# Kernel optimization log

Hardware: AMD Instinct MI355X
Metric: run time of the kernel (lower is better)

## Reference

```python
import jax, jax.numpy as jnp
import numpy as np

B, N, K = 4, 4096, 16
D_IN, D_T = 64, 128


def _linear_params(key, d_in, d_out, scale=0.02):
    kw, kb = jax.random.split(key)
    w = jax.random.normal(kw, (d_in, d_out), dtype=jnp.float32) * scale
    b = jax.random.normal(kb, (d_out,), dtype=jnp.float32) * scale
    return w, b


def setup_inputs() -> dict:
    key = jax.random.key(0)
    ks = jax.random.split(key, 12)
    x = jax.random.normal(ks[0], (B, N, D_IN), dtype=jnp.float32)
    pos = jax.random.normal(ks[1], (B, N, 3), dtype=jnp.float32)
    fc1_w, fc1_b = _linear_params(ks[2], D_IN, D_T)
    fc2_w, fc2_b = _linear_params(ks[3], D_T, D_IN)
    d1_w, d1_b = _linear_params(ks[4], 3, D_T)
    d2_w, d2_b = _linear_params(ks[5], D_T, D_T)
    g1_w, g1_b = _linear_params(ks[6], D_T, D_T)
    g2_w, g2_b = _linear_params(ks[7], D_T, D_T)
    wq = jax.random.normal(ks[8], (D_T, D_T), dtype=jnp.float32) * 0.02
    wk = jax.random.normal(ks[9], (D_T, D_T), dtype=jnp.float32) * 0.02
    wv = jax.random.normal(ks[10], (D_T, D_T), dtype=jnp.float32) * 0.02
    return dict(x=x, pos=pos, fc1_w=fc1_w, fc1_b=fc1_b, fc2_w=fc2_w, fc2_b=fc2_b,
                d1_w=d1_w, d1_b=d1_b, d2_w=d2_w, d2_b=d2_b,
                g1_w=g1_w, g1_b=g1_b, g2_w=g2_w, g2_b=g2_b,
                wq=wq, wk=wk, wv=wv)


def reference(x, pos, fc1_w, fc1_b, fc2_w, fc2_b, d1_w, d1_b, d2_w, d2_b,
              g1_w, g1_b, g2_w, g2_b, wq, wk, wv):
    # square_distance(pos, pos): [B, N, N]
    sq = jnp.sum(pos * pos, axis=-1)
    dists = sq[:, :, None] + sq[:, None, :] - 2.0 * jnp.einsum('bnc,bmc->bnm', pos, pos)
    knn_idx = jnp.argsort(dists, axis=-1)[:, :, :K]  # [B, N, K] int
    bidx = jnp.arange(B)[:, None, None]

    knn_pos = pos[bidx, knn_idx]                     # [B, N, K, 3]
    h = x @ fc1_w + fc1_b                            # [B, N, D_T]
    q = h @ wq                                       # [B, N, D_T]
    k = (h @ wk)[bidx, knn_idx]                      # [B, N, K, D_T]
    v = (h @ wv)[bidx, knn_idx]                      # [B, N, K, D_T]

    rel = pos[:, :, None, :] - knn_pos               # [B, N, K, 3]
    pos_enc = jax.nn.relu(rel @ d1_w + d1_b) @ d2_w + d2_b  # fc_delta

    a_in = q[:, :, None, :] - k + pos_enc
    attn = jax.nn.relu(a_in @ g1_w + g1_b) @ g2_w + g2_b    # fc_gamma
    attn = jax.nn.softmax(attn / np.sqrt(D_T).astype(np.float32), axis=-2)

    res = jnp.einsum('bmnf,bmnf->bmf', attn, v + pos_enc)   # [B, N, D_T]
    out = res @ fc2_w + fc2_b + x                           # [B, N, D_IN]
    return out, attn
```

## Files before the change

### kernel.cpp

```cpp
#include <hip/hip_runtime.h>
#include <float.h>

#define NPTS 4096
#define BN   16384
#define DT   128
#define DIN  64

typedef short v8s __attribute__((ext_vector_type(8)));
typedef float v4f __attribute__((ext_vector_type(4)));

__device__ __forceinline__ unsigned short f2bf(float f) {
    union { float f; unsigned u; } v; v.f = f;
    unsigned r = v.u + 0x7fff + ((v.u >> 16) & 1);
    return (unsigned short)(r >> 16);
}
__device__ __forceinline__ float bf2f(unsigned short s) {
    union { unsigned u; float f; } v; v.u = ((unsigned)s) << 16;
    return v.f;
}
__device__ __forceinline__ unsigned pack2(float lo, float hi) {
    unsigned r;
    asm("v_cvt_pk_bf16_f32 %0, %1, %2" : "=v"(r) : "v"(lo), "v"(hi));
    return r;
}

#define CSW(da,ia,db,ib) { bool sw_ = (da>db)||((da==db)&&(ia>ib)); \
    float td_=sw_?db:da, tD_=sw_?da:db; int ti_=sw_?ib:ia, tI_=sw_?ia:ib; \
    da=td_; db=tD_; ia=ti_; ib=tI_; }

__global__ __launch_bounds__(256) void front_kernel(
    const float* __restrict__ pos, const float* __restrict__ x,
    const float* __restrict__ fc1w, const float* __restrict__ fc1b,
    const float* __restrict__ wq, const float* __restrict__ wk,
    const float* __restrict__ wv,
    const float* __restrict__ d2w, const float* __restrict__ g1w,
    const float* __restrict__ g2w,
    float4* __restrict__ pos4, unsigned short* __restrict__ wB,
    int* __restrict__ knnb,
    unsigned short* __restrict__ qb, unsigned short* __restrict__ kb,
    unsigned short* __restrict__ vb) {
    __shared__ float smem[4096];
    int bid = blockIdx.x;
    int t = threadIdx.x;

    if (bid < 2048) {
        float (*scd)[256] = (float(*)[256])smem;
        int   (*sci)[256] = (int(*)[256])(smem + 2048);
        int lane = t & 63, w = t >> 6;
        int n0 = bid * 8 + w * 2;
        int base = n0 & ~(NPTS - 1);
        float pax = pos[n0*3], pay = pos[n0*3+1], paz = pos[n0*3+2];
        float paw = fmaf(paz, paz, fmaf(pay, pay, pax*pax));
        float pbx = pos[n0*3+3], pby = pos[n0*3+4], pbz = pos[n0*3+5];
        float pbw = fmaf(pbz, pbz, fmaf(pby, pby, pbx*pbx));

        float mina = FLT_MAX, minb = FLT_MAX;
        for (int m = lane; m < NPTS; m += 64) {
            const float* cp = &pos[(size_t)(base + m)*3];
            float cx = cp[0], cy = cp[1], cz = cp[2];
            float cw = fmaf(cz, cz, fmaf(cy, cy, cx*cx));
            float da = (paw + cw) - 2.0f * fmaf(paz, cz, fmaf(pay, cy, pax*cx));
            float db = (pbw + cw) - 2.0f * fmaf(pbz, cz, fmaf(pby, cy, pbx*cx));
            mina = fminf(mina, da); minb = fminf(minb, db);
        }
        float taua, taub;
        {
            float va = mina, vb_ = minb;
#pragma unroll
            for (int k = 2; k <= 64; k <<= 1) {
#pragma unroll
                for (int j = k >> 1; j > 0; j >>= 1) {
                    float oa = __shfl_xor(va, j, 64);
                    float ob = __shfl_xor(vb_, j, 64);
                    bool low = (lane & j) == 0;
                    bool asc = (lane & k) == 0;
                    va  = (low == asc) ? fminf(va, oa)  : fmaxf(va, oa);
                    vb_ = (low == asc) ? fminf(vb_, ob) : fmaxf(vb_, ob);
                }
            }
            taua = __shfl(va, 15, 64);
            taub = __shfl(vb_, 15, 64);
        }
        int ca = 0, cb = 0;
        for (int m = lane; m < NPTS; m += 64) {
            const float* cp = &pos[(size_t)(base + m)*3];
            float cx = cp[0], cy = cp[1], cz = cp[2];
            float cw = fmaf(cz, cz, fmaf(cy, cy, cx*cx));
            float da = (paw + cw) - 2.0f * fmaf(paz, cz, fmaf(pay, cy, pax*cx));
            float db = (pbw + cw) - 2.0f * fmaf(pbz, cz, fmaf(pby, cy, pbx*cx));
            bool ta = da <= taua, tb_ = db <= taub;
            unsigned long long ma = __ballot(ta), mb = __ballot(tb_);
            unsigned long long lower = (1ull << lane) - 1ull;
            if (ta) {
                int p_ = ca + __popcll(ma & lower);
                if (p_ < 256) { scd[w*2][p_] = da; sci[w*2][p_] = base + m; }
            }
            if (tb_) {
                int p_ = cb + __popcll(mb & lower);
                if (p_ < 256) { scd[w*2+1][p_] = db; sci[w*2+1][p_] = base + m; }
            }
            ca += __popcll(ma); cb += __popcll(mb);
        }
        if (ca > 256) ca = 256;
        if (cb > 256) cb = 256;
        for (int i = ca + lane; i < 256; i += 64) { scd[w*2][i]   = FLT_MAX; sci[w*2][i]   = 0x7fffffff; }
        for (int i = cb + lane; i < 256; i += 64) { scd[w*2+1][i] = FLT_MAX; sci[w*2+1][i] = 0x7fffffff; }
        __syncthreads();

        for (int pt = 0; pt < 2; pt++) {
            int s = w*2 + pt;
            float4 dv = *(const float4*)&scd[s][lane*4];
            int4   iv = *(const int4*)&sci[s][lane*4];
            CSW(dv.x, iv.x, dv.y, iv.y);
            CSW(dv.z, iv.z, dv.w, iv.w);
            CSW(dv.x, iv.x, dv.z, iv.z);
            CSW(dv.y, iv.y, dv.w, iv.w);
            CSW(dv.y, iv.y, dv.z, iv.z);
            int p = 0, myres = 0;
            for (int r = 0; r < 16; r++) {
                float hd = p==0 ? dv.x : p==1 ? dv.y : p==2 ? dv.z : p==3 ? dv.w : FLT_MAX;
                int   hi = p==0 ? iv.x : p==1 ? iv.y : p==2 ? iv.z : p==3 ? iv.w : 0x7fffffff;
                float bd = hd; int bi = hi;
                for (int off = 32; off; off >>= 1) {
                    float od = __shfl_xor(bd, off, 64);
                    int   oi = __shfl_xor(bi, off, 64);
                    if (od < bd || (od == bd && oi < bi)) { bd = od; bi = oi; }
                }
                if (hi == bi) p++;
                if (lane == r) myres = bi;
            }
            if (lane < 16) knnb[(n0 + pt)*16 + lane] = myres;
        }
    } else if (bid < 3072) {
        float (*xs)[64]  = (float(*)[64])smem;
        float (*hs)[128] = (float(*)[128])(smem + 1024);
        int rb = (bid - 2048) * 16;

        for (int i = t; i < 16*64; i += 256) xs[i>>6][i&63] = x[rb*64 + i];
        __syncthreads();

        int f4 = (t & 31) * 4;
        int r0 = (t >> 5) * 2, r1 = r0 + 1;
        float a0[4], a1[4];
#pragma unroll
        for (int jf = 0; jf < 4; jf++) { a0[jf] = fc1b[f4+jf]; a1[jf] = fc1b[f4+jf]; }
#pragma unroll 4
        for (int c = 0; c < 64; c += 4) {
            float s0[4], s1[4];
            *(float4*)s0 = *(const float4*)&xs[r0][c];
            *(float4*)s1 = *(const float4*)&xs[r1][c];
#pragma unroll
            for (int jc = 0; jc < 4; jc++) {
                float w[4];
                *(float4*)w = *(const float4*)&fc1w[(c+jc)*128 + f4];
#pragma unroll
                for (int jf = 0; jf < 4; jf++) {
                    a0[jf] = fmaf(s0[jc], w[jf], a0[jf]);
                    a1[jf] = fmaf(s1[jc], w[jf], a1[jf]);
                }
            }
        }
        *(float4*)&hs[r0][f4] = *(float4*)a0;
        *(float4*)&hs[r1][f4] = *(float4*)a1;
        __syncthreads();

        const float* Ws[3] = { wq, wk, wv };
        unsigned short* Os[3] = { qb, kb, vb };
        for (int mtx = 0; mtx < 3; mtx++) {
            const float* __restrict__ W = Ws[mtx];
#pragma unroll
            for (int jf = 0; jf < 4; jf++) { a0[jf] = 0.f; a1[jf] = 0.f; }
#pragma unroll 4
            for (int c = 0; c < 128; c += 4) {
                float s0[4], s1[4];
                *(float4*)s0 = *(const float4*)&hs[r0][c];
                *(float4*)s1 = *(const float4*)&hs[r1][c];
#pragma unroll
                for (int jc = 0; jc < 4; jc++) {
                    float w[4];
                    *(float4*)w = *(const float4*)&W[(c+jc)*128 + f4];
#pragma unroll
                    for (int jf = 0; jf < 4; jf++) {
                        a0[jf] = fmaf(s0[jc], w[jf], a0[jf]);
                        a1[jf] = fmaf(s1[jc], w[jf], a1[jf]);
                    }
                }
            }
            unsigned short* O = Os[mtx];
            uint2 s0v, s1v;
            s0v.x = pack2(a0[0], a0[1]); s0v.y = pack2(a0[2], a0[3]);
            s1v.x = pack2(a1[0], a1[1]); s1v.y = pack2(a1[2], a1[3]);
            *(uint2*)&O[(size_t)(rb+r0)*128 + f4] = s0v;
            *(uint2*)&O[(size_t)(rb+r1)*128 + f4] = s1v;
        }
    } else {
        int i = (bid - 3072) * 256 + t;
        if (i < BN) {
            float p0 = pos[i*3], p1 = pos[i*3+1], p2 = pos[i*3+2];
            pos4[i] = make_float4(p0, p1, p2, fmaf(p2, p2, fmaf(p1, p1, p0*p0)));
        } else {
            int e = i - BN; int m = e >> 14; e &= 16383;
            int k = e >> 7, n = e & 127;
            const float* W = (m == 0) ? d2w : (m == 1) ? g1w : g2w;
            float val = W[k*128 + n];
            int tile = n >> 4, nl = n & 15, ks = k >> 5, q = (k >> 3) & 3, j = k & 7;
            wB[m*16384 + ((tile*4 + ks)*64 + q*16 + nl)*8 + j] = f2bf(val);
        }
    }
}

__global__ __attribute__((amdgpu_waves_per_eu(4, 4)))
__launch_bounds__(1024) void fused_kernel(
    const float4* __restrict__ pos4, const int* __restrict__ knnb,
    const unsigned short* __restrict__ qb, const unsigned short* __restrict__ kb,
    const unsigned short* __restrict__ vb,
    const unsigned short* __restrict__ wB,
    const float* __restrict__ d1w, const float* __restrict__ d1b,
    const float* __restrict__ d2b, const float* __restrict__ g1b,
    const float* __restrict__ g2b,
    float* __restrict__ res, float* __restrict__ attn) {
    __shared__ unsigned short ws_[49152];
    __shared__ unsigned short tb[16][2048];
    int t = threadIdx.x;
    int lane = t & 63, w = t >> 6;
    int col = lane & 15, quad = lane >> 4;
    const float inv_s = 0.08838834764831845f;

    unsigned short* tw = &tb[w][0];
    float* twf = (float*)tw;

    {
        const uint4* src = (const uint4*)wB;
        uint4* dst = (uint4*)ws_;
        for (int i = t; i < 6144; i += 1024) dst[i] = src[i];
    }
    __syncthreads();

#pragma unroll
    for (int it = 0; it < 2; it++) {
        int n = (blockIdx.x * 16 + w) * 2 + it;
        {
            int jid = knnb[n*16 + col];

#pragma unroll
            for (int g = 0; g < 4; g++) {
                int kk2 = quad*4 + g;
                int jr2 = __shfl(jid, kk2);
                v8s kr = *(const v8s*)&kb[(size_t)jr2*128 + col*8];
                *(v8s*)&tw[kk2*128 + ((col ^ (kk2 & 7)) << 3)] = kr;
            }

            float4 pn = pos4[n];
            float4 pj = pos4[jid];
            float dx = pn.x - pj.x, dy = pn.y - pj.y, dz = pn.z - pj.z;

            v8s af[4];
#pragma unroll
            for (int ks = 0; ks < 4; ks++) {
                int fb = ks*32 + quad*8;
                float w0[8], w1[8], w2[8], bb[8];
                *(float4*)&w0[0] = *(const float4*)&d1w[fb];
                *(float4*)&w0[4] = *(const float4*)&d1w[fb+4];
                *(float4*)&w1[0] = *(const float4*)&d1w[128+fb];
                *(float4*)&w1[4] = *(const float4*)&d1w[128+fb+4];
                *(float4*)&w2[0] = *(const float4*)&d1w[256+fb];
                *(float4*)&w2[4] = *(const float4*)&d1w[256+fb+4];
                *(float4*)&bb[0] = *(const float4*)&d1b[fb];
                *(float4*)&bb[4] = *(const float4*)&d1b[fb+4];
                union { v8s s; unsigned u[4]; } afu;
#pragma unroll
                for (int j2 = 0; j2 < 4; j2++) {
                    float h0 = fmaf(dz, w2[j2*2],   fmaf(dy, w1[j2*2],   fmaf(dx, w0[j2*2],   bb[j2*2])));
                    float h1 = fmaf(dz, w2[j2*2+1], fmaf(dy, w1[j2*2+1], fmaf(dx, w0[j2*2+1], bb[j2*2+1])));
                    afu.u[j2] = pack2(fmaxf(h0, 0.0f), fmaxf(h1, 0.0f));
                }
                af[ks] = afu.s;
            }

            v8s frag[4];
            unsigned peP[16];

            {
                unsigned wo = 0; asm volatile("" : "+v"(wo));
#pragma unroll
                for (int tt = 0; tt < 8; tt++) {
                    v4f acc = {0.f, 0.f, 0.f, 0.f};
#pragma unroll
                    for (int ks = 0; ks < 4; ks++) {
                        v8s b = *(const v8s*)&ws_[wo + ((tt*4 + ks) << 9) + (lane << 3)];
                        acc = __builtin_amdgcn_mfma_f32_16x16x32_bf16(af[ks], b, acc, 0, 0, 0);
                    }
                    int cg = tt*16 + col;
                    float bias = d2b[cg];
                    float qv = bf2f(qb[(size_t)n*128 + cg]);
                    float pe0 = 0.f, pe1 = 0.f;
#pragma unroll
                    for (int r = 0; r < 4; r++) {
                        int kk = quad*4 + r;
                        int pidx = kk*128 + ((((cg >> 3) ^ (kk & 7))) << 3) + (cg & 6);
                        unsigned kp = *(const unsigned*)&tw[pidx];
                        float kv = bf2f((unsigned short)((lane & 1) ? (kp >> 16) : (kp & 0xffff)));
                        float pe = acc[r] + bias;
                        if (r == 0) pe0 = pe;
                        if (r == 1) { peP[tt*2]   = pack2(pe0, pe); }
                        if (r == 2) pe1 = pe;
                        if (r == 3) { peP[tt*2+1] = pack2(pe1, pe); }
                        float a  = qv - kv + pe;
                        float o = __shfl_xor(a, 1);
                        if ((lane & 1) == 0) *(unsigned*)&tw[pidx] = pack2(a, o);
                    }
                }
#pragma unroll
                for (int ks = 0; ks < 4; ks++)
                    frag[ks] = *(const v8s*)&tw[col*128 + ((((ks*4 + quad) ^ (col & 7))) << 3)];
            }

            {
                unsigned wo = 16384; asm volatile("" : "+v"(wo));
#pragma unroll
                for (int tt = 0; tt < 8; tt++) {
                    v4f acc = {0.f, 0.f, 0.f, 0.f};
#pragma unroll
                    for (int ks = 0; ks < 4; ks++) {
                        v8s b = *(const v8s*)&ws_[wo + ((tt*4 + ks) << 9) + (lane << 3)];
                        acc = __builtin_amdgcn_mfma_f32_16x16x32_bf16(frag[ks], b, acc, 0, 0, 0);
                    }
                    float bias = g1b[tt*16 + col];
#pragma unroll
                    for (int r = 0; r < 4; r++) {
                        float h = fmaxf(acc[r] + bias, 0.0f);
                        float o = __shfl_xor(h, 1);
                        if ((lane & 1) == 0) {
                            int kk = quad*4 + r;
                            int cg = tt*16 + col;
                            int idx = kk*128 + ((((cg >> 3) ^ (kk & 7))) << 3) + (cg & 7);
                            *(unsigned*)&tw[idx] = pack2(h, o);
                        }
                    }
                }
#pragma unroll
                for (int ks = 0; ks < 4; ks++)
                    frag[ks] = *(const v8s*)&tw[col*128 + ((((ks*4 + quad) ^ (col & 7))) << 3)];
            }

            {
#pragma unroll
                for (int g = 0; g < 4; g++) {
                    int kk2 = quad*4 + g;
                    int jr2 = __shfl(jid, kk2);
                    v8s vr = *(const v8s*)&vb[(size_t)jr2*128 + col*8];
                    *(v8s*)&tw[kk2*128 + ((col ^ (kk2 & 7)) << 3)] = vr;
                }

                unsigned wo = 32768; asm volatile("" : "+v"(wo));
                float av[8][4];
#pragma unroll
                for (int tt = 0; tt < 8; tt++) {
                    v4f acc = {0.f, 0.f, 0.f, 0.f};
#pragma unroll
                    for (int ks = 0; ks < 4; ks++) {
                        v8s b = *(const v8s*)&ws_[wo + ((tt*4 + ks) << 9) + (lane << 3)];
                        acc = __builtin_amdgcn_mfma_f32_16x16x32_bf16(frag[ks], b, acc, 0, 0, 0);
                    }
                    int cg = tt*16 + col;
                    float bias = g2b[cg];
                    float l[4];
                    float mx = -FLT_MAX;
#pragma unroll
                    for (int r = 0; r < 4; r++) {
                        l[r] = (acc[r] + bias) * inv_s;
                        mx = fmaxf(mx, l[r]);
                    }
                    mx = fmaxf(mx, __shfl_xor(mx, 16));
                    mx = fmaxf(mx, __shfl_xor(mx, 32));
                    float s = 0.f;
#pragma unroll
                    for (int r = 0; r < 4; r++) { l[r] = __expf(l[r] - mx); s += l[r]; }
                    s += __shfl_xor(s, 16);
                    s += __shfl_xor(s, 32);
                    float rs = 1.0f / s;
                    float rp = 0.f;
#pragma unroll
                    for (int r = 0; r < 4; r++) {
                        int kk = quad*4 + r;
                        int pidx = kk*128 + ((((cg >> 3) ^ (kk & 7))) << 3) + (cg & 6);
                        unsigned vp = *(const unsigned*)&tw[pidx];
                        float vv = bf2f((unsigned short)((lane & 1) ? (vp >> 16) : (vp & 0xffff)));
                        unsigned pp = peP[tt*2 + (r >> 1)];
                        float pe = bf2f((unsigned short)((r & 1) ? (pp >> 16) : (pp & 0xffff)));
                        float a_ = l[r] * rs;
                        av[tt][r] = a_;
                        rp = fmaf(a_, vv + pe, rp);
                    }
                    rp += __shfl_xor(rp, 16);
                    rp += __shfl_xor(rp, 32);
                    if (lane < 16) res[(size_t)n*128 + cg] = rp;
                }

#pragma unroll
                for (int h = 0; h < 2; h++) {
#pragma unroll
                    for (int tt2 = 0; tt2 < 4; tt2++) {
#pragma unroll
                        for (int r = 0; r < 4; r++) {
                            int kk = quad*4 + r;
                            twf[kk*64 + ((tt2*16 + col) ^ ((kk & 4) << 2))] = av[h*4 + tt2][r];
                        }
                    }
#pragma unroll
                    for (int s4 = 0; s4 < 4; s4++) {
                        int kk = s4*4 + quad;
                        int c4 = col*4;
                        float4 a4 = *(const float4*)&twf[kk*64 + (c4 ^ ((kk & 4) << 2))];
                        *(float4*)&attn[(size_t)(n*16 + kk)*128 + h*64 + c4] = a4;
                    }
                }
            }
        }
    }
}

__global__ __launch_bounds__(256) void epi_kernel(
    const float* __restrict__ res, const float* __restrict__ fc2w,
    const float* __restrict__ fc2b, const float* __restrict__ x,
    float* __restrict__ out) {
    __shared__ float fw[128][64];
    __shared__ float rs[16][128];
    int t = threadIdx.x;
    int rb = blockIdx.x * 16;
    for (int i = t; i < 8192; i += 256) fw[i >> 6][i & 63] = fc2w[i];
    for (int i = t; i < 2048; i += 256) rs[i >> 7][i & 127] = res[(size_t)rb*128 + i];
    __syncthreads();

    int o = t & 63, g = t >> 6;
#pragma unroll
    for (int rr = 0; rr < 4; rr++) {
        int lr = rr*4 + g;
        int n = rb + lr;
        float a0 = 0.f, a1 = 0.f, a2 = 0.f, a3 = 0.f;
#pragma unroll 8
        for (int c = 0; c < 128; c += 4) {
            a0 = fmaf(rs[lr][c],   fw[c][o],   a0);
            a1 = fmaf(rs[lr][c+1], fw[c+1][o], a1);
            a2 = fmaf(rs[lr][c+2], fw[c+2][o], a2);
            a3 = fmaf(rs[lr][c+3], fw[c+3][o], a3);
        }
        out[(size_t)n*64 + o] = (a0 + a1) + (a2 + a3) + fc2b[o] + x[(size_t)n*64 + o];
    }
}

extern "C" void kernel_launch(void* const* d_in, const int* in_sizes, int n_in,
                              void* d_out, int out_size, void* d_ws, size_t ws_size,
                              hipStream_t stream) {
    (void)in_sizes; (void)n_in; (void)out_size; (void)ws_size;
    const float* x    = (const float*)d_in[0];
    const float* pos  = (const float*)d_in[1];
    const float* fc1w = (const float*)d_in[2];
    const float* fc1b = (const float*)d_in[3];
    const float* fc2w = (const float*)d_in[4];
    const float* fc2b = (const float*)d_in[5];
    const float* d1w  = (const float*)d_in[6];
    const float* d1b  = (const float*)d_in[7];
    const float* d2w  = (const float*)d_in[8];
    const float* d2b  = (const float*)d_in[9];
    const float* g1w  = (const float*)d_in[10];
    const float* g1b  = (const float*)d_in[11];
    const float* g2w  = (const float*)d_in[12];
    const float* g2b  = (const float*)d_in[13];
    const float* wq   = (const float*)d_in[14];
    const float* wk   = (const float*)d_in[15];
    const float* wv   = (const float*)d_in[16];

    float* out      = (float*)d_out;
    float* attn_out = out + (size_t)BN * DIN;

    char* W = (char*)d_ws;
    float4*         pos4  = (float4*)(W + 0);
    unsigned short* wB    = (unsigned short*)(W + 262144);
    int*            knnb  = (int*)(W + 376832);
    unsigned short* qb    = (unsigned short*)(W + 1441792);
    unsigned short* kb    = (unsigned short*)(W + 5636096);
    unsigned short* vb    = (unsigned short*)(W + 9830400);
    float*          res   = (float*)(W + 14024704);

    front_kernel<<<3328, 256, 0, stream>>>(pos, x, fc1w, fc1b, wq, wk, wv,
                                           d2w, g1w, g2w,
                                           pos4, wB, knnb, qb, kb, vb);
    fused_kernel<<<512, 1024, 0, stream>>>(pos4, knnb, qb, kb, vb, wB, d1w, d1b,
                                           d2b, g1b, g2b, res, attn_out);
    epi_kernel<<<1024, 256, 0, stream>>>(res, fc2w, fc2b, x, out);
}
```

Measured before the change: 435.8 us.

## Split KNN into own kernel and stage candidate positions in LDS

Moves the KNN search out of the combined front kernel into a dedicated kernel, with the remaining front work in a separate launch. Each KNN block first loads all 4096 batch positions into shared memory as float4 with precomputed squared norm, so the two scan passes read LDS instead of strided global loads and recompute no norms. This costs 64KB of LDS per block, which limits occupancy, and adds an extra kernel launch.

```diff
diff --git a/kernel.cpp b/kernel.cpp
--- a/kernel.cpp
+++ b/kernel.cpp
@@ -28,7 +28,102 @@
     float td_=sw_?db:da, tD_=sw_?da:db; int ti_=sw_?ib:ia, tI_=sw_?ia:ib; \
     da=td_; db=tD_; ia=ti_; ib=tI_; }
 
-__global__ __launch_bounds__(256) void front_kernel(
+__global__ __launch_bounds__(256) void knn_kernel(const float* __restrict__ pos,
+                                                  int* __restrict__ knnb) {
+    __shared__ float4 pc[NPTS];
+    __shared__ float scd[8][256];
+    __shared__ int   sci[8][256];
+    int t = threadIdx.x, lane = t & 63, w = t >> 6;
+    int n0 = blockIdx.x * 8 + w * 2;
+    int base = n0 & ~(NPTS - 1);
+
+    for (int p = t; p < NPTS; p += 256) {
+        const float* cp = &pos[(size_t)(base + p)*3];
+        float cx = cp[0], cy = cp[1], cz = cp[2];
+        pc[p] = make_float4(cx, cy, cz, fmaf(cz, cz, fmaf(cy, cy, cx*cx)));
+    }
+
+    float pax = pos[n0*3], pay = pos[n0*3+1], paz = pos[n0*3+2];
+    float paw = fmaf(paz, paz, fmaf(pay, pay, pax*pax));
+    float pbx = pos[n0*3+3], pby = pos[n0*3+4], pbz = pos[n0*3+5];
+    float pbw = fmaf(pbz, pbz, fmaf(pby, pby, pbx*pbx));
+    __syncthreads();
+
+    float mina = FLT_MAX, minb = FLT_MAX;
+    for (int m = lane; m < NPTS; m += 64) {
+        float4 c = pc[m];
+        float da = (paw + c.w) - 2.0f * fmaf(paz, c.z, fmaf(pay, c.y, pax*c.x));
+        float db = (pbw + c.w) - 2.0f * fmaf(pbz, c.z, fmaf(pby, c.y, pbx*c.x));
+        mina = fminf(mina, da); minb = fminf(minb, db);
+    }
+    float taua, taub;
+    {
+        float va = mina, vb_ = minb;
+#pragma unroll
+        for (int k = 2; k <= 64; k <<= 1) {
+#pragma unroll
+            for (int j = k >> 1; j > 0; j >>= 1) {
+                float oa = __shfl_xor(va, j, 64);
+                float ob = __shfl_xor(vb_, j, 64);
+                bool low = (lane & j) == 0;
+                bool asc = (lane & k) == 0;
+                va  = (low == asc) ? fminf(va, oa)  : fmaxf(va, oa);
+                vb_ = (low == asc) ? fminf(vb_, ob) : fmaxf(vb_, ob);
+            }
+        }
+        taua = __shfl(va, 15, 64);
+        taub = __shfl(vb_, 15, 64);
+    }
+    int ca = 0, cb = 0;
+    for (int m = lane; m < NPTS; m += 64) {
+        float4 c = pc[m];
+        float da = (paw + c.w) - 2.0f * fmaf(paz, c.z, fmaf(pay, c.y, pax*c.x));
+        float db = (pbw + c.w) - 2.0f * fmaf(pbz, c.z, fmaf(pby, c.y, pbx*c.x));
+        bool ta = da <= taua, tb_ = db <= taub;
+        unsigned long long ma = __ballot(ta), mb = __ballot(tb_);
+        unsigned long long lower = (1ull << lane) - 1ull;
+        if (ta) {
+            int p_ = ca + __popcll(ma & lower);
+            if (p_ < 256) { scd[w*2][p_] = da; sci[w*2][p_] = base + m; }
+        }
+        if (tb_) {
+            int p_ = cb + __popcll(mb & lower);
+            if (p_ < 256) { scd[w*2+1][p_] = db; sci[w*2+1][p_] = base + m; }
+        }
+        ca += __popcll(ma); cb += __popcll(mb);
+    }
+    if (ca > 256) ca = 256;
+    if (cb > 256) cb = 256;
+    for (int i = ca + lane; i < 256; i += 64) { scd[w*2][i]   = FLT_MAX; sci[w*2][i]   = 0x7fffffff; }
+    for (int i = cb + lane; i < 256; i += 64) { scd[w*2+1][i] = FLT_MAX; sci[w*2+1][i] = 0x7fffffff; }
+
+    for (int pt = 0; pt < 2; pt++) {
+        int s = w*2 + pt;
+        float4 dv = *(const float4*)&scd[s][lane*4];
+        int4   iv = *(const int4*)&sci[s][lane*4];
+        CSW(dv.x, iv.x, dv.y, iv.y);
+        CSW(dv.z, iv.z, dv.w, iv.w);
+        CSW(dv.x, iv.x, dv.z, iv.z);
+        CSW(dv.y, iv.y, dv.w, iv.w);
+        CSW(dv.y, iv.y, dv.z, iv.z);
+        int p = 0, myres = 0;
+        for (int r = 0; r < 16; r++) {
+            float hd = p==0 ? dv.x : p==1 ? dv.y : p==2 ? dv.z : p==3 ? dv.w : FLT_MAX;
+            int   hi = p==0 ? iv.x : p==1 ? iv.y : p==2 ? iv.z : p==3 ? iv.w : 0x7fffffff;
+            float bd = hd; int bi = hi;
+            for (int off = 32; off; off >>= 1) {
+                float od = __shfl_xor(bd, off, 64);
+                int   oi = __shfl_xor(bi, off, 64);
+                if (od < bd || (od == bd && oi < bi)) { bd = od; bi = oi; }
+            }
+            if (hi == bi) p++;
+            if (lane == r) myres = bi;
+        }
+        if (lane < 16) knnb[(n0 + pt)*16 + lane] = myres;
+    }
+}
+
+__global__ __launch_bounds__(256) void fp_kernel(
     const float* __restrict__ pos, const float* __restrict__ x,
     const float* __restrict__ fc1w, const float* __restrict__ fc1b,
     const float* __restrict__ wq, const float* __restrict__ wk,
@@ -36,105 +131,16 @@
     const float* __restrict__ d2w, const float* __restrict__ g1w,
     const float* __restrict__ g2w,
     float4* __restrict__ pos4, unsigned short* __restrict__ wB,
-    int* __restrict__ knnb,
     unsigned short* __restrict__ qb, unsigned short* __restrict__ kb,
     unsigned short* __restrict__ vb) {
-    __shared__ float smem[4096];
+    __shared__ float smem[3072];
     int bid = blockIdx.x;
     int t = threadIdx.x;
 
-    if (bid < 2048) {
-        float (*scd)[256] = (float(*)[256])smem;
-        int   (*sci)[256] = (int(*)[256])(smem + 2048);
-        int lane = t & 63, w = t >> 6;
-        int n0 = bid * 8 + w * 2;
-        int base = n0 & ~(NPTS - 1);
-        float pax = pos[n0*3], pay = pos[n0*3+1], paz = pos[n0*3+2];
-        float paw = fmaf(paz, paz, fmaf(pay, pay, pax*pax));
-        float pbx = pos[n0*3+3], pby = pos[n0*3+4], pbz = pos[n0*3+5];
-        float pbw = fmaf(pbz, pbz, fmaf(pby, pby, pbx*pbx));
-
-        float mina = FLT_MAX, minb = FLT_MAX;
-        for (int m = lane; m < NPTS; m += 64) {
-            const float* cp = &pos[(size_t)(base + m)*3];
-            float cx = cp[0], cy = cp[1], cz = cp[2];
-            float cw = fmaf(cz, cz, fmaf(cy, cy, cx*cx));
-            float da = (paw + cw) - 2.0f * fmaf(paz, cz, fmaf(pay, cy, pax*cx));
-            float db = (pbw + cw) - 2.0f * fmaf(pbz, cz, fmaf(pby, cy, pbx*cx));
-            mina = fminf(mina, da); minb = fminf(minb, db);
-        }
-        float taua, taub;
-        {
-            float va = mina, vb_ = minb;
-#pragma unroll
-            for (int k = 2; k <= 64; k <<= 1) {
-#pragma unroll
-                for (int j = k >> 1; j > 0; j >>= 1) {
-                    float oa = __shfl_xor(va, j, 64);
-                    float ob = __shfl_xor(vb_, j, 64);
-                    bool low = (lane & j) == 0;
-                    bool asc = (lane & k) == 0;
-                    va  = (low == asc) ? fminf(va, oa)  : fmaxf(va, oa);
-                    vb_ = (low == asc) ? fminf(vb_, ob) : fmaxf(vb_, ob);
-                }
-            }
-            taua = __shfl(va, 15, 64);
-            taub = __shfl(vb_, 15, 64);
-        }
-        int ca = 0, cb = 0;
-        for (int m = lane; m < NPTS; m += 64) {
-            const float* cp = &pos[(size_t)(base + m)*3];
-            float cx = cp[0], cy = cp[1], cz = cp[2];
-            float cw = fmaf(cz, cz, fmaf(cy, cy, cx*cx));
-            float da = (paw + cw) - 2.0f * fmaf(paz, cz, fmaf(pay, cy, pax*cx));
-            float db = (pbw + cw) - 2.0f * fmaf(pbz, cz, fmaf(pby, cy, pbx*cx));
-            bool ta = da <= taua, tb_ = db <= taub;
-            unsigned long long ma = __ballot(ta), mb = __ballot(tb_);
-            unsigned long long lower = (1ull << lane) - 1ull;
-            if (ta) {
-                int p_ = ca + __popcll(ma & lower);
-                if (p_ < 256) { scd[w*2][p_] = da; sci[w*2][p_] = base + m; }
-            }
-            if (tb_) {
-                int p_ = cb + __popcll(mb & lower);
-                if (p_ < 256) { scd[w*2+1][p_] = db; sci[w*2+1][p_] = base + m; }
-            }
-            ca += __popcll(ma); cb += __popcll(mb);
-        }
-        if (ca > 256) ca = 256;
-        if (cb > 256) cb = 256;
-        for (int i = ca + lane; i < 256; i += 64) { scd[w*2][i]   = FLT_MAX; sci[w*2][i]   = 0x7fffffff; }
-        for (int i = cb + lane; i < 256; i += 64) { scd[w*2+1][i] = FLT_MAX; sci[w*2+1][i] = 0x7fffffff; }
-        __syncthreads();
-
-        for (int pt = 0; pt < 2; pt++) {
-            int s = w*2 + pt;
-            float4 dv = *(const float4*)&scd[s][lane*4];
-            int4   iv = *(const int4*)&sci[s][lane*4];
-            CSW(dv.x, iv.x, dv.y, iv.y);
-            CSW(dv.z, iv.z, dv.w, iv.w);
-            CSW(dv.x, iv.x, dv.z, iv.z);
-            CSW(dv.y, iv.y, dv.w, iv.w);
-            CSW(dv.y, iv.y, dv.z, iv.z);
-            int p = 0, myres = 0;
-            for (int r = 0; r < 16; r++) {
-                float hd = p==0 ? dv.x : p==1 ? dv.y : p==2 ? dv.z : p==3 ? dv.w : FLT_MAX;
-                int   hi = p==0 ? iv.x : p==1 ? iv.y : p==2 ? iv.z : p==3 ? iv.w : 0x7fffffff;
-                float bd = hd; int bi = hi;
-                for (int off = 32; off; off >>= 1) {
-                    float od = __shfl_xor(bd, off, 64);
-                    int   oi = __shfl_xor(bi, off, 64);
-                    if (od < bd || (od == bd && oi < bi)) { bd = od; bi = oi; }
-                }
-                if (hi == bi) p++;
-                if (lane == r) myres = bi;
-            }
-            if (lane < 16) knnb[(n0 + pt)*16 + lane] = myres;
-        }
-    } else if (bid < 3072) {
+    if (bid < 1024) {
         float (*xs)[64]  = (float(*)[64])smem;
         float (*hs)[128] = (float(*)[128])(smem + 1024);
-        int rb = (bid - 2048) * 16;
+        int rb = bid * 16;
 
         for (int i = t; i < 16*64; i += 256) xs[i>>6][i&63] = x[rb*64 + i];
         __syncthreads();
@@ -194,7 +200,7 @@
             *(uint2*)&O[(size_t)(rb+r1)*128 + f4] = s1v;
         }
     } else {
-        int i = (bid - 3072) * 256 + t;
+        int i = (bid - 1024) * 256 + t;
         if (i < BN) {
             float p0 = pos[i*3], p1 = pos[i*3+1], p2 = pos[i*3+2];
             pos4[i] = make_float4(p0, p1, p2, fmaf(p2, p2, fmaf(p1, p1, p0*p0)));
@@ -483,9 +489,9 @@
     unsigned short* vb    = (unsigned short*)(W + 9830400);
     float*          res   = (float*)(W + 14024704);
 
-    front_kernel<<<3328, 256, 0, stream>>>(pos, x, fc1w, fc1b, wq, wk, wv,
-                                           d2w, g1w, g2w,
-                                           pos4, wB, knnb, qb, kb, vb);
+    knn_kernel<<<2048, 256, 0, stream>>>(pos, knnb);
+    fp_kernel<<<1280, 256, 0, stream>>>(pos, x, fc1w, fc1b, wq, wk, wv,
+                                        d2w, g1w, g2w, pos4, wB, qb, kb, vb);
     fused_kernel<<<512, 1024, 0, stream>>>(pos4, knnb, qb, kb, vb, wB, d1w, d1b,
                                            d2b, g1b, g2b, res, attn_out);
     epi_kernel<<<1024, 256, 0, stream>>>(res, fc2w, fc2b, x, out);
```

Result: slower. 479.2 us (+9.9%).
